# Optimization experiments

Measured on AMD Instinct MI355X. Metric: run time of the kernel, lower is better.

The kernel has to match this reference:

```python
import jax, jax.numpy as jnp
import numpy as np

N_NODES = 100000
N_EDGES = 3200000
F_IN, H_ENC, H_GCN, H_Q, A_DIM = 128, 128, 128, 256, 10


def setup_inputs() -> dict:
    key = jax.random.key(0)
    ks = jax.random.split(key, 8)
    s = lambda d: 1.0 / np.sqrt(d)
    return {
        "x": jax.random.normal(ks[0], (N_NODES, F_IN), jnp.float32),
        "edge_index": jax.random.randint(ks[1], (2, N_EDGES), 0, N_NODES, jnp.int64),
        "W_enc": jax.random.normal(ks[2], (F_IN, H_ENC), jnp.float32) * s(F_IN),
        "b_enc": jnp.zeros((H_ENC,), jnp.float32),
        "W_gcn": jax.random.normal(ks[3], (H_ENC, H_GCN), jnp.float32) * s(H_ENC),
        "b_gcn": jnp.zeros((H_GCN,), jnp.float32),
        "W1": jax.random.normal(ks[4], (H_GCN, H_Q), jnp.float32) * s(H_GCN),
        "b1": jnp.zeros((H_Q,), jnp.float32),
        "W2": jax.random.normal(ks[5], (H_Q, A_DIM), jnp.float32) * s(H_Q),
        "b2": jnp.zeros((A_DIM,), jnp.float32),
    }


def gcn_conv(x, edge_index, W, b):
    # Standard GCNConv: D^{-1/2} (A + I) D^{-1/2} X W + b, symmetric norm with self-loops.
    n = x.shape[0]
    src, dst = edge_index[0], edge_index[1]
    xw = x @ W  # [N, H]
    deg = jnp.ones((n,), xw.dtype).at[dst].add(1.0)  # in-degree + self-loop
    dinv = jax.lax.rsqrt(deg)
    coef = dinv[src] * dinv[dst]  # [E]
    msg = xw[src] * coef[:, None]  # [E, H] gather-scale
    agg = jax.ops.segment_sum(msg, dst, num_segments=n)  # scatter-add
    agg = agg + xw * (dinv * dinv)[:, None]  # self-loop contribution
    return agg + b


def reference(x, edge_index, W_enc, b_enc, W_gcn, b_gcn, W1, b1, W2, b2):
    h = jax.nn.relu(x @ W_enc + b_enc)              # Encoder: Linear + ReLU
    h = jax.nn.relu(gcn_conv(h, edge_index, W_gcn, b_gcn))  # GCNConv + ReLU
    q = jax.nn.relu(h @ W1 + b1) @ W2 + b2          # Q_Net MLP
    return q
```

## Files before the change

kernel.cpp:

```cpp
#include <hip/hip_runtime.h>

#define N_NODES 100000
constexpr int F     = 128;
constexpr int NB    = (N_NODES + 63) / 64;
constexpr int BCAP  = 2560;
constexpr int LCAP  = 80;
constexpr int CHUNK = 32768;
constexpr int PADN  = N_NODES;

typedef __attribute__((ext_vector_type(8))) short short8;
typedef __attribute__((ext_vector_type(4))) float f32x4;
typedef __attribute__((ext_vector_type(4))) short short4v;

__device__ inline short f2bf(float v) {
    union { float f; unsigned u; } x; x.f = v;
    unsigned r = (x.u + 0x7fff + ((x.u >> 16) & 1)) >> 16;
    return (short)r;
}
__device__ inline float lo_bf(unsigned v) {
    union { unsigned u; float f; } x; x.u = v << 16; return x.f;
}
__device__ inline float hi_bf(unsigned v) {
    union { unsigned u; float f; } x; x.u = v & 0xffff0000u; return x.f;
}

__global__ __launch_bounds__(256) void prep_kernel(const float* __restrict__ W_enc,
                                                   const float* __restrict__ W_gcn,
                                                   const float* __restrict__ W1,
                                                   const float* __restrict__ W2,
                                                   short* __restrict__ Wte,
                                                   short* __restrict__ Wtg,
                                                   short* __restrict__ Wt1,
                                                   short* __restrict__ W2t,
                                                   int* __restrict__ bcr) {
    int idx = blockIdx.x * 256 + threadIdx.x;
    if (idx < 16384) { int h = idx >> 7, k = idx & 127; Wte[idx] = f2bf(W_enc[k * 128 + h]); return; }
    idx -= 16384;
    if (idx < 16384) { int h = idx >> 7, k = idx & 127; Wtg[idx] = f2bf(W_gcn[k * 128 + h]); return; }
    idx -= 16384;
    if (idx < 32768) { int h = idx >> 7, k = idx & 127; Wt1[idx] = f2bf(W1[k * 256 + h]); return; }
    idx -= 32768;
    if (idx < 4096)  { int n = idx >> 8, k = idx & 255; W2t[idx] = (n < 10) ? f2bf(W2[k * 10 + n]) : (short)0; return; }
    idx -= 4096;
    if (idx < NB) bcr[idx] = 0;
}

__global__ __launch_bounds__(256) void part_kernel(const int* __restrict__ src,
                                                   const int* __restrict__ dst,
                                                   int* __restrict__ bcur,
                                                   int* __restrict__ part, int E) {
    __shared__ int cnt[NB];
    __shared__ int base[NB];
    for (int b = threadIdx.x; b < NB; b += 256) cnt[b] = 0;
    __syncthreads();
    const int e0 = blockIdx.x * CHUNK;
    const int e1 = min(e0 + CHUNK, E);
#pragma unroll 4
    for (int e = e0 + threadIdx.x; e < e1; e += 256)
        atomicAdd(&cnt[dst[e] >> 6], 1);
    __syncthreads();
    for (int b = threadIdx.x; b < NB; b += 256) {
        int c = cnt[b];
        base[b] = c ? atomicAdd(&bcur[b], c) : 0;
        cnt[b] = 0;
    }
    __syncthreads();
#pragma unroll 4
    for (int e = e0 + threadIdx.x; e < e1; e += 256) {
        int d = dst[e];
        int b = d >> 6;
        int idx = base[b] + atomicAdd(&cnt[b], 1);
        if (idx < BCAP) part[b * BCAP + idx] = src[e] | ((d & 63) << 17);
    }
}

__global__ __launch_bounds__(256) void gemmA_kernel(const float* __restrict__ x,
                                                    const short* __restrict__ Wte,
                                                    const short* __restrict__ Wtg,
                                                    const float* __restrict__ b_enc,
                                                    const int* __restrict__ bcur,
                                                    const int* __restrict__ part,
                                                    short* __restrict__ xs) {
    __shared__ int deg_l[64];
    __shared__ short h_l[4][16][136];
    const int b = blockIdx.x;
    if (threadIdx.x < 64) deg_l[threadIdx.x] = 0;
    __syncthreads();
    const int cnt = min(bcur[b], BCAP);
    const int* p = part + (size_t)b * BCAP;
#pragma unroll 4
    for (int i = threadIdx.x; i < cnt; i += 256)
        atomicAdd(&deg_l[(p[i] >> 17) & 63], 1);

    const int wave = threadIdx.x >> 6;
    const int lane = threadIdx.x & 63;
    const int quad = lane >> 4;
    const int l16  = lane & 15;
    const int node0 = b * 64 + wave * 16;
    int nrow = node0 + l16;
    const bool valid = nrow < N_NODES;
    if (!valid) nrow = N_NODES - 1;

    f32x4 acc[8] = {};
#pragma unroll
    for (int kc = 0; kc < 4; ++kc) {
        const float* ap = x + (size_t)nrow * 128 + kc * 32 + quad * 8;
        float4 f0 = *reinterpret_cast<const float4*>(ap);
        float4 f1 = *reinterpret_cast<const float4*>(ap + 4);
        short8 xfrag;
        xfrag.s0 = f2bf(f0.x); xfrag.s1 = f2bf(f0.y); xfrag.s2 = f2bf(f0.z); xfrag.s3 = f2bf(f0.w);
        xfrag.s4 = f2bf(f1.x); xfrag.s5 = f2bf(f1.y); xfrag.s6 = f2bf(f1.z); xfrag.s7 = f2bf(f1.w);
#pragma unroll
        for (int t = 0; t < 8; ++t) {
            short8 wfrag = *reinterpret_cast<const short8*>(Wte + (size_t)(t * 16 + l16) * 128 + kc * 32 + quad * 8);
            acc[t] = __builtin_amdgcn_mfma_f32_16x16x32_bf16(wfrag, xfrag, acc[t], 0, 0, 0);
        }
    }
#pragma unroll
    for (int t = 0; t < 8; ++t) {
        short4v o;
#pragma unroll
        for (int r = 0; r < 4; ++r)
            ((short*)&o)[r] = f2bf(fmaxf(acc[t][r] + b_enc[t * 16 + quad * 4 + r], 0.f));
        *reinterpret_cast<short4v*>(&h_l[wave][l16][t * 16 + quad * 4]) = o;
    }
    __syncthreads();

    const float dvn = rsqrtf(1.f + (float)deg_l[wave * 16 + l16]);
    f32x4 acc2[8] = {};
#pragma unroll
    for (int kc = 0; kc < 4; ++kc) {
        short8 xfrag = *reinterpret_cast<const short8*>(&h_l[wave][l16][kc * 32 + quad * 8]);
#pragma unroll
        for (int t = 0; t < 8; ++t) {
            short8 wfrag = *reinterpret_cast<const short8*>(Wtg + (size_t)(t * 16 + l16) * 128 + kc * 32 + quad * 8);
            acc2[t] = __builtin_amdgcn_mfma_f32_16x16x32_bf16(wfrag, xfrag, acc2[t], 0, 0, 0);
        }
    }
    const int srow = node0 + l16;
#pragma unroll
    for (int t = 0; t < 8; ++t) {
        short4v o;
#pragma unroll
        for (int r = 0; r < 4; ++r)
            ((short*)&o)[r] = valid ? f2bf(acc2[t][r] * dvn) : (short)0;
        *reinterpret_cast<short4v*>(xs + (size_t)(valid ? srow : srow) * 128 + t * 16 + quad * 4) = o;
    }
}

__global__ __launch_bounds__(256) void agg_kernel(const short* __restrict__ xs,
                                                  const int* __restrict__ bcur,
                                                  const int* __restrict__ part,
                                                  const float* __restrict__ bg,
                                                  short* __restrict__ h2) {
    __shared__ int csr_l[64 * LCAP];
    __shared__ int cur[64];
    const int b = blockIdx.x;
    if (threadIdx.x < 64) cur[threadIdx.x] = 0;
    __syncthreads();
    const int cnt = min(bcur[b], BCAP);
    const int* p = part + (size_t)b * BCAP;
#pragma unroll 4
    for (int i = threadIdx.x; i < cnt; i += 256) {
        int v = p[i];
        int ld = (v >> 17) & 63;
        int pos = atomicAdd(&cur[ld], 1);
        if (pos < LCAP) csr_l[ld * LCAP + pos] = v & 0x1FFFF;
    }
    __syncthreads();

    const int wave = threadIdx.x >> 6;
    const int lane = threadIdx.x & 63;
    const unsigned* xsu = reinterpret_cast<const unsigned*>(xs);
    for (int t = 0; t < 16; ++t) {
        const int ld = wave * 16 + t;
        const int node = b * 64 + ld;
        if (node >= N_NODES) break;

        const int dtrue = cur[ld];
        const int d = min(dtrue, LCAP);
        const float dv = rsqrtf(1.f + (float)dtrue);

        int s0 = PADN, s1 = PADN;
        if (lane < d)      s0 = csr_l[ld * LCAP + lane];
        if (lane + 64 < d) s1 = csr_l[ld * LCAP + lane + 64];

        float ax = 0.f, ay = 0.f;
        const int dpad = (d + 7) & ~7;
        const int n0 = dpad < 64 ? dpad : 64;
        for (int j0 = 0; j0 < n0; j0 += 8) {
#pragma unroll
            for (int u = 0; u < 8; ++u) {
                int sj = __shfl(s0, j0 + u, 64);
                unsigned v = xsu[((size_t)sj << 6) + lane];
                ax += lo_bf(v);
                ay += hi_bf(v);
            }
        }
        for (int j0 = 64; j0 < dpad; j0 += 8) {
#pragma unroll
            for (int u = 0; u < 8; ++u) {
                int sj = __shfl(s1, j0 + u - 64, 64);
                unsigned v = xsu[((size_t)sj << 6) + lane];
                ax += lo_bf(v);
                ay += hi_bf(v);
            }
        }
        unsigned vs = xsu[((size_t)node << 6) + lane];
        ax += lo_bf(vs);
        ay += hi_bf(vs);
        ax = fmaxf(fmaf(ax, dv, bg[lane * 2 + 0]), 0.f);
        ay = fmaxf(fmaf(ay, dv, bg[lane * 2 + 1]), 0.f);
        unsigned o = (unsigned)(unsigned short)f2bf(ax) | ((unsigned)(unsigned short)f2bf(ay) << 16);
        *(reinterpret_cast<unsigned*>(h2 + ((size_t)node << 7)) + lane) = o;
    }
}

__global__ __launch_bounds__(256) void gemmB_kernel(const short* __restrict__ h2,
                                                    const short* __restrict__ Wt1,
                                                    const short* __restrict__ W2t,
                                                    const float* __restrict__ b1,
                                                    const float* __restrict__ b2,
                                                    float* __restrict__ q) {
    __shared__ short hq_l[4][16][264];
    const int wave = threadIdx.x >> 6;
    const int lane = threadIdx.x & 63;
    const int quad = lane >> 4;
    const int l16  = lane & 15;
    const int node0 = blockIdx.x * 64 + wave * 16;
    int nrow = node0 + l16;
    if (nrow >= N_NODES) nrow = N_NODES - 1;

    f32x4 acc[16] = {};
#pragma unroll
    for (int kc = 0; kc < 4; ++kc) {
        short8 xfrag = *reinterpret_cast<const short8*>(h2 + (size_t)nrow * 128 + kc * 32 + quad * 8);
#pragma unroll
        for (int t = 0; t < 16; ++t) {
            short8 wfrag = *reinterpret_cast<const short8*>(Wt1 + (size_t)(t * 16 + l16) * 128 + kc * 32 + quad * 8);
            acc[t] = __builtin_amdgcn_mfma_f32_16x16x32_bf16(wfrag, xfrag, acc[t], 0, 0, 0);
        }
    }
#pragma unroll
    for (int t = 0; t < 16; ++t) {
        short4v o;
#pragma unroll
        for (int r = 0; r < 4; ++r)
            ((short*)&o)[r] = f2bf(fmaxf(acc[t][r] + b1[t * 16 + quad * 4 + r], 0.f));
        *reinterpret_cast<short4v*>(&hq_l[wave][l16][t * 16 + quad * 4]) = o;
    }

    f32x4 a2 = {};
#pragma unroll
    for (int kc = 0; kc < 8; ++kc) {
        short8 afrag = *reinterpret_cast<const short8*>(&hq_l[wave][l16][kc * 32 + quad * 8]);
        short8 bfrag = *reinterpret_cast<const short8*>(W2t + (size_t)l16 * 256 + kc * 32 + quad * 8);
        a2 = __builtin_amdgcn_mfma_f32_16x16x32_bf16(afrag, bfrag, a2, 0, 0, 0);
    }
    if (l16 < 10) {
        float bv = b2[l16];
#pragma unroll
        for (int r = 0; r < 4; ++r) {
            int nd = node0 + quad * 4 + r;
            if (nd < N_NODES) q[(size_t)nd * 10 + l16] = a2[r] + bv;
        }
    }
}

extern "C" void kernel_launch(void* const* d_in, const int* in_sizes, int n_in,
                              void* d_out, int out_size, void* d_ws, size_t ws_size,
                              hipStream_t stream) {
    const float* x     = (const float*)d_in[0];
    const int*   ei    = (const int*)d_in[1];
    const float* W_enc = (const float*)d_in[2];
    const float* b_enc = (const float*)d_in[3];
    const float* W_gcn = (const float*)d_in[4];
    const float* b_gcn = (const float*)d_in[5];
    const float* W1    = (const float*)d_in[6];
    const float* b1    = (const float*)d_in[7];
    const float* W2    = (const float*)d_in[8];
    const float* b2    = (const float*)d_in[9];
    float* q = (float*)d_out;

    const int E = in_sizes[1] / 2;
    const int* srcv = ei;
    const int* dstv = ei + E;

    char* ws = (char*)d_ws;
    const size_t XSB = (size_t)(NB * 64) * 128 * sizeof(short);
    short* xs  = (short*)(ws);
    short* h2  = (short*)(ws + XSB);
    int*   part= (int*)  (ws + 2 * XSB);
    char*  tail = ws + 2 * XSB + (size_t)NB * BCAP * sizeof(int);
    int*   bcr = (int*)(tail);
    short* Wte = (short*)(tail + 8192);
    short* Wtg = (short*)(tail + 8192 + 32768);
    short* Wt1 = (short*)(tail + 8192 + 65536);
    short* W2t = (short*)(tail + 8192 + 131072);

    prep_kernel<<<279, 256, 0, stream>>>(W_enc, W_gcn, W1, W2, Wte, Wtg, Wt1, W2t, bcr);
    part_kernel<<<(E + CHUNK - 1) / CHUNK, 256, 0, stream>>>(srcv, dstv, bcr, part, E);
    gemmA_kernel<<<NB, 256, 0, stream>>>(x, Wte, Wtg, b_enc, bcr, part, xs);
    agg_kernel<<<NB, 256, 0, stream>>>(xs, bcr, part, b_gcn, h2);
    gemmB_kernel<<<NB, 256, 0, stream>>>(h2, Wt1, W2t, b1, b2, q);
}
```

Measured before the change: 463.7 us.

## Split aggregation wave into two edge halves with 8-byte loads; shrink partition chunks

The aggregation kernel now has each half-wave handle alternate neighbours. Each lane loads 8 bytes (4 bf16 features) instead of 4, neighbour indices are read straight from LDS instead of via shuffles, padding entries are pre-filled, and the two halves are combined with a cross-lane xor shuffle. This doubles the number of neighbour rows in flight per wave, to raise memory-level parallelism on the gather. Separately, the partition kernel uses 512-thread blocks with a quarter-size chunk, giving many more blocks but also more global atomics on the bucket counters.

```diff
diff --git a/kernel.cpp b/kernel.cpp
--- a/kernel.cpp
+++ b/kernel.cpp
@@ -5,7 +5,7 @@
 constexpr int NB    = (N_NODES + 63) / 64;
 constexpr int BCAP  = 2560;
 constexpr int LCAP  = 80;
-constexpr int CHUNK = 32768;
+constexpr int CHUNK = 8192;
 constexpr int PADN  = N_NODES;
 
 typedef __attribute__((ext_vector_type(8))) short short8;
@@ -45,28 +45,28 @@
     if (idx < NB) bcr[idx] = 0;
 }
 
-__global__ __launch_bounds__(256) void part_kernel(const int* __restrict__ src,
+__global__ __launch_bounds__(512) void part_kernel(const int* __restrict__ src,
                                                    const int* __restrict__ dst,
                                                    int* __restrict__ bcur,
                                                    int* __restrict__ part, int E) {
     __shared__ int cnt[NB];
     __shared__ int base[NB];
-    for (int b = threadIdx.x; b < NB; b += 256) cnt[b] = 0;
+    for (int b = threadIdx.x; b < NB; b += 512) cnt[b] = 0;
     __syncthreads();
     const int e0 = blockIdx.x * CHUNK;
     const int e1 = min(e0 + CHUNK, E);
 #pragma unroll 4
-    for (int e = e0 + threadIdx.x; e < e1; e += 256)
+    for (int e = e0 + threadIdx.x; e < e1; e += 512)
         atomicAdd(&cnt[dst[e] >> 6], 1);
     __syncthreads();
-    for (int b = threadIdx.x; b < NB; b += 256) {
+    for (int b = threadIdx.x; b < NB; b += 512) {
         int c = cnt[b];
         base[b] = c ? atomicAdd(&bcur[b], c) : 0;
         cnt[b] = 0;
     }
     __syncthreads();
 #pragma unroll 4
-    for (int e = e0 + threadIdx.x; e < e1; e += 256) {
+    for (int e = e0 + threadIdx.x; e < e1; e += 512) {
         int d = dst[e];
         int b = d >> 6;
         int idx = base[b] + atomicAdd(&cnt[b], 1);
@@ -144,7 +144,7 @@
 #pragma unroll
         for (int r = 0; r < 4; ++r)
             ((short*)&o)[r] = valid ? f2bf(acc2[t][r] * dvn) : (short)0;
-        *reinterpret_cast<short4v*>(xs + (size_t)(valid ? srow : srow) * 128 + t * 16 + quad * 4) = o;
+        *reinterpret_cast<short4v*>(xs + (size_t)srow * 128 + t * 16 + quad * 4) = o;
     }
 }
 
@@ -156,63 +156,70 @@
     __shared__ int csr_l[64 * LCAP];
     __shared__ int cur[64];
     const int b = blockIdx.x;
-    if (threadIdx.x < 64) cur[threadIdx.x] = 0;
+    const int tid = threadIdx.x;
+    if (tid < 64) cur[tid] = 0;
     __syncthreads();
     const int cnt = min(bcur[b], BCAP);
     const int* p = part + (size_t)b * BCAP;
 #pragma unroll 4
-    for (int i = threadIdx.x; i < cnt; i += 256) {
+    for (int i = tid; i < cnt; i += 256) {
         int v = p[i];
         int ld = (v >> 17) & 63;
         int pos = atomicAdd(&cur[ld], 1);
         if (pos < LCAP) csr_l[ld * LCAP + pos] = v & 0x1FFFF;
     }
     __syncthreads();
-
-    const int wave = threadIdx.x >> 6;
-    const int lane = threadIdx.x & 63;
-    const unsigned* xsu = reinterpret_cast<const unsigned*>(xs);
+    if (tid < 64) {
+        int d = min(cur[tid], LCAP);
+        int dp = (d + 7) & ~7;
+        for (int k = d; k < dp; ++k) csr_l[tid * LCAP + k] = PADN;
+    }
+    __syncthreads();
+
+    const int wave = tid >> 6;
+    const int lane = tid & 63;
+    const int half = lane >> 5;
+    const int fl   = lane & 31;
+    const uint2* xs2 = reinterpret_cast<const uint2*>(xs);
+    const float4 bg4 = reinterpret_cast<const float4*>(bg)[fl];
+
     for (int t = 0; t < 16; ++t) {
         const int ld = wave * 16 + t;
         const int node = b * 64 + ld;
         if (node >= N_NODES) break;
 
         const int dtrue = cur[ld];
-        const int d = min(dtrue, LCAP);
+        const int dpad = (min(dtrue, LCAP) + 7) & ~7;
         const float dv = rsqrtf(1.f + (float)dtrue);
-
-        int s0 = PADN, s1 = PADN;
-        if (lane < d)      s0 = csr_l[ld * LCAP + lane];
-        if (lane + 64 < d) s1 = csr_l[ld * LCAP + lane + 64];
-
-        float ax = 0.f, ay = 0.f;
-        const int dpad = (d + 7) & ~7;
-        const int n0 = dpad < 64 ? dpad : 64;
-        for (int j0 = 0; j0 < n0; j0 += 8) {
-#pragma unroll
-            for (int u = 0; u < 8; ++u) {
-                int sj = __shfl(s0, j0 + u, 64);
-                unsigned v = xsu[((size_t)sj << 6) + lane];
-                ax += lo_bf(v);
-                ay += hi_bf(v);
+        const int* cl = csr_l + ld * LCAP;
+
+        float a0 = 0.f, a1 = 0.f, a2 = 0.f, a3 = 0.f;
+        for (int j = 0; j < dpad; j += 8) {
+#pragma unroll
+            for (int u = 0; u < 4; ++u) {
+                int sj = cl[j + u * 2 + half];
+                uint2 v = xs2[((size_t)sj << 5) + fl];
+                a0 += lo_bf(v.x); a1 += hi_bf(v.x);
+                a2 += lo_bf(v.y); a3 += hi_bf(v.y);
             }
         }
-        for (int j0 = 64; j0 < dpad; j0 += 8) {
-#pragma unroll
-            for (int u = 0; u < 8; ++u) {
-                int sj = __shfl(s1, j0 + u - 64, 64);
-                unsigned v = xsu[((size_t)sj << 6) + lane];
-                ax += lo_bf(v);
-                ay += hi_bf(v);
-            }
-        }
-        unsigned vs = xsu[((size_t)node << 6) + lane];
-        ax += lo_bf(vs);
-        ay += hi_bf(vs);
-        ax = fmaxf(fmaf(ax, dv, bg[lane * 2 + 0]), 0.f);
-        ay = fmaxf(fmaf(ay, dv, bg[lane * 2 + 1]), 0.f);
-        unsigned o = (unsigned)(unsigned short)f2bf(ax) | ((unsigned)(unsigned short)f2bf(ay) << 16);
-        *(reinterpret_cast<unsigned*>(h2 + ((size_t)node << 7)) + lane) = o;
+        a0 += __shfl_xor(a0, 32, 64);
+        a1 += __shfl_xor(a1, 32, 64);
+        a2 += __shfl_xor(a2, 32, 64);
+        a3 += __shfl_xor(a3, 32, 64);
+        uint2 vs = xs2[((size_t)node << 5) + fl];
+        a0 += lo_bf(vs.x); a1 += hi_bf(vs.x);
+        a2 += lo_bf(vs.y); a3 += hi_bf(vs.y);
+        a0 = fmaxf(fmaf(a0, dv, bg4.x), 0.f);
+        a1 = fmaxf(fmaf(a1, dv, bg4.y), 0.f);
+        a2 = fmaxf(fmaf(a2, dv, bg4.z), 0.f);
+        a3 = fmaxf(fmaf(a3, dv, bg4.w), 0.f);
+        if (lane < 32) {
+            uint2 o;
+            o.x = (unsigned)(unsigned short)f2bf(a0) | ((unsigned)(unsigned short)f2bf(a1) << 16);
+            o.y = (unsigned)(unsigned short)f2bf(a2) | ((unsigned)(unsigned short)f2bf(a3) << 16);
+            reinterpret_cast<uint2*>(h2)[((size_t)node << 5) + fl] = o;
+        }
     }
 }
 
@@ -299,7 +306,7 @@
     short* W2t = (short*)(tail + 8192 + 131072);
 
     prep_kernel<<<279, 256, 0, stream>>>(W_enc, W_gcn, W1, W2, Wte, Wtg, Wt1, W2t, bcr);
-    part_kernel<<<(E + CHUNK - 1) / CHUNK, 256, 0, stream>>>(srcv, dstv, bcr, part, E);
+    part_kernel<<<(E + CHUNK - 1) / CHUNK, 512, 0, stream>>>(srcv, dstv, bcr, part, E);
     gemmA_kernel<<<NB, 256, 0, stream>>>(x, Wte, Wtg, b_enc, bcr, part, xs);
     agg_kernel<<<NB, 256, 0, stream>>>(xs, bcr, part, b_gcn, h2);
     gemmB_kernel<<<NB, 256, 0, stream>>>(h2, Wt1, W2t, b1, b2, q);
```

After: 407.8 us. -12.1%, faster.
